# Kernel tuning notes

Hardware: AMD Instinct MI355X
Metric: run time of the kernel (lower is better)

Reference implementation:

```python
import jax, jax.numpy as jnp
import numpy as np

HEAD_DIM = 64
SCALE = HEAD_DIM ** -0.5
NUM_HEADS = 16


def setup_inputs() -> dict:
    key = jax.random.key(0)
    k1, k2, k3, k4 = jax.random.split(key, 4)
    dim = 1024
    query = jax.random.normal(k1, (8, 512, dim), dtype=jnp.float32)
    memory = jax.random.normal(k2, (8, 512, dim), dtype=jnp.float32)
    # nn.Linear weights are [out, in]; scale like default init
    W_Q = jax.random.normal(k3, (dim, dim), dtype=jnp.float32) * (dim ** -0.5)
    W_K = jax.random.normal(k4, (dim, dim), dtype=jnp.float32) * (dim ** -0.5)
    return {"query": query, "memory": memory, "W_Q": W_Q, "W_K": W_K}


def reference(query, memory, W_Q, W_K):
    # Q: [K, Lq, E], K: [B, Lk, E]  (E = H * D)
    Q = query @ W_Q.T
    Km = memory @ W_K.T
    Kb, Lq, E = Q.shape
    Bb, Lk, _ = Km.shape
    Qh = Q.reshape(Kb, Lq, NUM_HEADS, HEAD_DIM).transpose(0, 2, 1, 3)  # K H q D
    Kh = Km.reshape(Bb, Lk, NUM_HEADS, HEAD_DIM).transpose(0, 2, 1, 3)  # B H k D
    # logits: [B, K, H, q, k]
    logits = jnp.einsum('ahqd,bhkd->bahqk', Qh, Kh) * SCALE
    energies = jax.nn.logsumexp(logits, axis=-2) / SCALE  # [B, K, H, k]
    energies = energies.mean(axis=1)  # [B, H, k]
    return energies
```

## Files before the change

### kernel.cpp

```cpp
#include <hip/hip_runtime.h>
#include <hip/hip_bf16.h>

typedef short short8 __attribute__((ext_vector_type(8)));
typedef float f32x4 __attribute__((ext_vector_type(4)));
typedef unsigned short u16;

__device__ __forceinline__ unsigned short f2bf(float f) {
  unsigned int u = __float_as_uint(f);
  u += 0x7fffu + ((u >> 16) & 1u);
  return (unsigned short)(u >> 16);
}

__device__ __forceinline__ void glds16(const void* g, void* l) {
  __builtin_amdgcn_global_load_lds(
      (const __attribute__((address_space(1))) unsigned int*)g,
      (__attribute__((address_space(3))) unsigned int*)l, 16, 0, 0);
}

__device__ __forceinline__ void drain_then_sync() {
  __builtin_amdgcn_s_waitcnt(0);
  __syncthreads();
}

__global__ __launch_bounds__(256) void prep(const float4* __restrict__ q,
                                            const float4* __restrict__ m,
                                            const float4* __restrict__ wq,
                                            const float4* __restrict__ wk,
                                            ushort4* __restrict__ qb,
                                            ushort4* __restrict__ mb,
                                            ushort4* __restrict__ wqb,
                                            ushort4* __restrict__ wkb,
                                            float4* __restrict__ out0) {
  const int i = blockIdx.x * 256 + threadIdx.x;
  const float c = 0.18033688011112042f;
  if (i < 1048576) {
    float4 v = q[i];
    ushort4 o; o.x = f2bf(v.x); o.y = f2bf(v.y); o.z = f2bf(v.z); o.w = f2bf(v.w);
    qb[i] = o;
  } else if (i < 2097152) {
    float4 v = m[i - 1048576];
    ushort4 o; o.x = f2bf(v.x); o.y = f2bf(v.y); o.z = f2bf(v.z); o.w = f2bf(v.w);
    mb[i - 1048576] = o;
  } else if (i < 2359296) {
    float4 v = wq[i - 2097152];
    ushort4 o; o.x = f2bf(v.x * c); o.y = f2bf(v.y * c); o.z = f2bf(v.z * c); o.w = f2bf(v.w * c);
    wqb[i - 2097152] = o;
  } else if (i < 2621440) {
    float4 v = wk[i - 2359296];
    ushort4 o; o.x = f2bf(v.x); o.y = f2bf(v.y); o.z = f2bf(v.z); o.w = f2bf(v.w);
    wkb[i - 2359296] = o;
  } else if (i < 2637824) {
    out0[i - 2621440] = (float4){0.f, 0.f, 0.f, 0.f};
  }
}

__global__ __launch_bounds__(512) void gemm_db(const u16* __restrict__ A0,
                                               const u16* __restrict__ B0,
                                               u16* __restrict__ C0,
                                               const u16* __restrict__ A1,
                                               const u16* __restrict__ B1,
                                               u16* __restrict__ C1) {
  __shared__ u16 As[2][128 * 64];
  __shared__ u16 Bs[2][128 * 64];
  const int zz = blockIdx.x & 1;
  const u16* A = zz ? A1 : A0;
  const u16* B = zz ? B1 : B0;
  u16* C = zz ? C1 : C0;
  const int t = threadIdx.x;
  const int lane = t & 63, wave = t >> 6;
  const int l15 = lane & 15, quad = lane >> 4;
  const int mb = (blockIdx.x >> 1) * 128;
  const int nb = blockIdx.y * 128;
  const int wm = (wave & 1) * 64;
  const int wn = (wave >> 1) * 32;

  const int srow = lane >> 3;
  const int scol = ((lane & 7) ^ srow) * 8;
  const int sw = l15 & 7;

  f32x4 acc[4][2];
#pragma unroll
  for (int i = 0; i < 4; i++)
#pragma unroll
    for (int j = 0; j < 2; j++) acc[i][j] = (f32x4){0.f, 0.f, 0.f, 0.f};

#pragma unroll
  for (int j = 0; j < 2; j++) {
    const int g = wave * 2 + j;
    glds16(A + (size_t)(mb + g * 8 + srow) * 1024 + scol, &As[0][g * 512 + lane * 8]);
    glds16(B + (size_t)(nb + g * 8 + srow) * 1024 + scol, &Bs[0][g * 512 + lane * 8]);
  }

  for (int it = 0; it < 16; ++it) {
    drain_then_sync();
    if (it < 15) {
      const int kb = (it + 1) * 64, bf_ = (it + 1) & 1;
#pragma unroll
      for (int j = 0; j < 2; j++) {
        const int g = wave * 2 + j;
        glds16(A + (size_t)(mb + g * 8 + srow) * 1024 + kb + scol, &As[bf_][g * 512 + lane * 8]);
        glds16(B + (size_t)(nb + g * 8 + srow) * 1024 + kb + scol, &Bs[bf_][g * 512 + lane * 8]);
      }
    }
    const u16* as = As[it & 1];
    const u16* bs = Bs[it & 1];
#pragma unroll
    for (int kk = 0; kk < 2; kk++) {
      const int cb = kk * 4;
      short8 af[4], bfr[2];
#pragma unroll
      for (int mi = 0; mi < 4; mi++)
        af[mi] = *(const short8*)&as[(wm + mi * 16 + l15) * 64 + ((cb + quad) ^ sw) * 8];
#pragma unroll
      for (int ni = 0; ni < 2; ni++)
        bfr[ni] = *(const short8*)&bs[(wn + ni * 16 + l15) * 64 + ((cb + quad) ^ sw) * 8];
#pragma unroll
      for (int mi = 0; mi < 4; mi++)
#pragma unroll
        for (int ni = 0; ni < 2; ni++)
          acc[mi][ni] = __builtin_amdgcn_mfma_f32_16x16x32_bf16(
              af[mi], bfr[ni], acc[mi][ni], 0, 0, 0);
    }
  }

#pragma unroll
  for (int mi = 0; mi < 4; mi++)
#pragma unroll
    for (int r = 0; r < 4; r++) {
      const int row = mb + wm + mi * 16 + quad * 4 + r;
      const size_t base = (size_t)row * 1024 + nb + wn;
#pragma unroll
      for (int ni = 0; ni < 2; ni++)
        C[base + ni * 16 + l15] = f2bf(acc[mi][ni][r]);
    }
}

__global__ __launch_bounds__(256) void attn_lse2(const u16* __restrict__ Qp,
                                                 const u16* __restrict__ Kp,
                                                 float* __restrict__ out) {
  __shared__ u16 qs[2][64 * 64];
  const int t = threadIdx.x;
  const int lane = t & 63, wave = t >> 6;
  const int l15 = lane & 15, quad = lane >> 4;
  const int kt = blockIdx.x & 1, aa = blockIdx.x >> 1;
  const int h = blockIdx.y, b = blockIdx.z;
  const int kwave = kt * 256 + wave * 64;

  short8 klo[4], khi[4];
#pragma unroll
  for (int tt = 0; tt < 4; tt++) {
    const short8* kg = (const short8*)(Kp + (size_t)(b * 512 + kwave + tt * 16 + l15) * 1024
                                       + h * 64 + quad * 8);
    klo[tt] = kg[0];
    khi[tt] = kg[4];
  }

  const int srow = lane >> 3;
  const int scol = ((lane & 7) ^ srow) * 8;
  const u16* qbase = Qp + (size_t)(aa * 512) * 1024 + h * 64;

  const int sw = l15 & 7;
  const int colLo = (quad ^ sw) * 8;
  const int colHi = ((4 + quad) ^ sw) * 8;
  const int rrow = l15 * 64;

  float cs0 = 0.f, cs1 = 0.f, cs2 = 0.f, cs3 = 0.f;

#pragma unroll
  for (int j = 0; j < 2; j++) {
    const int mi_ = wave * 2 + j;
    glds16(qbase + (size_t)(mi_ * 8 + srow) * 1024 + scol, &qs[0][mi_ * 512 + lane * 8]);
  }

  for (int i = 0; i < 8; i++) {
    drain_then_sync();
    if (i < 7) {
#pragma unroll
      for (int j = 0; j < 2; j++) {
        const int mi_ = wave * 2 + j;
        glds16(qbase + (size_t)((i + 1) * 64 + mi_ * 8 + srow) * 1024 + scol,
               &qs[(i + 1) & 1][mi_ * 512 + lane * 8]);
      }
    }
    const u16* buf = qs[i & 1];
#pragma unroll
    for (int qt = 0; qt < 4; qt++) {
      short8 alo = *(const short8*)&buf[qt * 1024 + rrow + colLo];
      short8 ahi = *(const short8*)&buf[qt * 1024 + rrow + colHi];
      f32x4 ac0 = (f32x4){0.f, 0.f, 0.f, 0.f};
      f32x4 ac1 = ac0, ac2 = ac0, ac3 = ac0;
      ac0 = __builtin_amdgcn_mfma_f32_16x16x32_bf16(alo, klo[0], ac0, 0, 0, 0);
      ac0 = __builtin_amdgcn_mfma_f32_16x16x32_bf16(ahi, khi[0], ac0, 0, 0, 0);
      ac1 = __builtin_amdgcn_mfma_f32_16x16x32_bf16(alo, klo[1], ac1, 0, 0, 0);
      ac1 = __builtin_amdgcn_mfma_f32_16x16x32_bf16(ahi, khi[1], ac1, 0, 0, 0);
      ac2 = __builtin_amdgcn_mfma_f32_16x16x32_bf16(alo, klo[2], ac2, 0, 0, 0);
      ac2 = __builtin_amdgcn_mfma_f32_16x16x32_bf16(ahi, khi[2], ac2, 0, 0, 0);
      ac3 = __builtin_amdgcn_mfma_f32_16x16x32_bf16(alo, klo[3], ac3, 0, 0, 0);
      ac3 = __builtin_amdgcn_mfma_f32_16x16x32_bf16(ahi, khi[3], ac3, 0, 0, 0);
#pragma unroll
      for (int r = 0; r < 4; r++) {
        cs0 += __builtin_amdgcn_exp2f(ac0[r]);
        cs1 += __builtin_amdgcn_exp2f(ac1[r]);
        cs2 += __builtin_amdgcn_exp2f(ac2[r]);
        cs3 += __builtin_amdgcn_exp2f(ac3[r]);
      }
    }
  }
  cs0 += __shfl_xor(cs0, 16); cs0 += __shfl_xor(cs0, 32);
  cs1 += __shfl_xor(cs1, 16); cs1 += __shfl_xor(cs1, 32);
  cs2 += __shfl_xor(cs2, 16); cs2 += __shfl_xor(cs2, 32);
  cs3 += __shfl_xor(cs3, 16); cs3 += __shfl_xor(cs3, 32);
  const float v = quad == 0 ? cs0 : quad == 1 ? cs1 : quad == 2 ? cs2 : cs3;
  atomicAdd(out + (size_t)b * 8192 + h * 512 + kwave + quad * 16 + l15, __logf(v));
}

extern "C" void kernel_launch(void* const* d_in, const int* in_sizes, int n_in,
                              void* d_out, int out_size, void* d_ws, size_t ws_size,
                              hipStream_t stream) {
  const float* query  = (const float*)d_in[0];
  const float* memory = (const float*)d_in[1];
  const float* wq     = (const float*)d_in[2];
  const float* wk     = (const float*)d_in[3];
  float* out = (float*)d_out;

  char* ws = (char*)d_ws;
  const size_t MB = 1024 * 1024;
  u16* qb  = (u16*)(ws);
  u16* mb_ = (u16*)(ws + 8  * MB);
  u16* wqb = (u16*)(ws + 16 * MB);
  u16* wkb = (u16*)(ws + 18 * MB);
  u16* Qp  = (u16*)(ws + 20 * MB);
  u16* Kp  = (u16*)(ws + 28 * MB);

  prep<<<10304, 256, 0, stream>>>((const float4*)query, (const float4*)memory,
                                  (const float4*)wq, (const float4*)wk,
                                  (ushort4*)qb, (ushort4*)mb_, (ushort4*)wqb,
                                  (ushort4*)wkb, (float4*)d_out);
  gemm_db<<<dim3(64, 8), 512, 0, stream>>>(qb, wqb, Qp, mb_, wkb, Kp);
  attn_lse2<<<dim3(16, 16, 8), 256, 0, stream>>>(Qp, Kp, out);
}
```

Measured before the change: 147.3 us.

## Load Q in two 256-row chunks instead of double-buffered 64-row tiles

Replaces the 8-step double-buffered 64-row Q pipeline with two phases. Each phase loads 256 Q rows into a 32KB LDS buffer, waits once, then computes. This cuts the number of barriers and waitcnt drains from eight to two, but it loses the overlap between loads and compute within each phase and quadruples LDS use per block, which may lower occupancy. The exp accumulators are also split into four independent lanes per column to break the serial add dependency chain.

```diff
diff --git a/kernel.cpp b/kernel.cpp
--- a/kernel.cpp
+++ b/kernel.cpp
@@ -138,7 +138,7 @@
 __global__ __launch_bounds__(256) void attn_lse2(const u16* __restrict__ Qp,
                                                  const u16* __restrict__ Kp,
                                                  float* __restrict__ out) {
-  __shared__ u16 qs[2][64 * 64];
+  __shared__ u16 qs[256 * 64];
   const int t = threadIdx.x;
   const int lane = t & 63, wave = t >> 6;
   const int l15 = lane & 15, quad = lane >> 4;
@@ -164,48 +164,49 @@
   const int colHi = ((4 + quad) ^ sw) * 8;
   const int rrow = l15 * 64;
 
-  float cs0 = 0.f, cs1 = 0.f, cs2 = 0.f, cs3 = 0.f;
-
-#pragma unroll
-  for (int j = 0; j < 2; j++) {
-    const int mi_ = wave * 2 + j;
-    glds16(qbase + (size_t)(mi_ * 8 + srow) * 1024 + scol, &qs[0][mi_ * 512 + lane * 8]);
-  }
-
-  for (int i = 0; i < 8; i++) {
+  f32x4 csv0 = (f32x4){0.f, 0.f, 0.f, 0.f};
+  f32x4 csv1 = csv0, csv2 = csv0, csv3 = csv0;
+
+  for (int s = 0; s < 2; ++s) {
+    if (s) __syncthreads();
+#pragma unroll
+    for (int j = 0; j < 8; ++j) {
+      const int g = wave * 8 + j;
+      glds16(qbase + (size_t)(s * 256 + g * 8 + srow) * 1024 + scol,
+             &qs[g * 512 + lane * 8]);
+    }
     drain_then_sync();
-    if (i < 7) {
-#pragma unroll
-      for (int j = 0; j < 2; j++) {
-        const int mi_ = wave * 2 + j;
-        glds16(qbase + (size_t)((i + 1) * 64 + mi_ * 8 + srow) * 1024 + scol,
-               &qs[(i + 1) & 1][mi_ * 512 + lane * 8]);
+
+    for (int ii = 0; ii < 4; ++ii) {
+      const u16* buf = qs + ii * 4096;
+#pragma unroll
+      for (int qt = 0; qt < 4; ++qt) {
+        short8 alo = *(const short8*)&buf[qt * 1024 + rrow + colLo];
+        short8 ahi = *(const short8*)&buf[qt * 1024 + rrow + colHi];
+        f32x4 ac0 = (f32x4){0.f, 0.f, 0.f, 0.f};
+        f32x4 ac1 = ac0, ac2 = ac0, ac3 = ac0;
+        ac0 = __builtin_amdgcn_mfma_f32_16x16x32_bf16(alo, klo[0], ac0, 0, 0, 0);
+        ac0 = __builtin_amdgcn_mfma_f32_16x16x32_bf16(ahi, khi[0], ac0, 0, 0, 0);
+        ac1 = __builtin_amdgcn_mfma_f32_16x16x32_bf16(alo, klo[1], ac1, 0, 0, 0);
+        ac1 = __builtin_amdgcn_mfma_f32_16x16x32_bf16(ahi, khi[1], ac1, 0, 0, 0);
+        ac2 = __builtin_amdgcn_mfma_f32_16x16x32_bf16(alo, klo[2], ac2, 0, 0, 0);
+        ac2 = __builtin_amdgcn_mfma_f32_16x16x32_bf16(ahi, khi[2], ac2, 0, 0, 0);
+        ac3 = __builtin_amdgcn_mfma_f32_16x16x32_bf16(alo, klo[3], ac3, 0, 0, 0);
+        ac3 = __builtin_amdgcn_mfma_f32_16x16x32_bf16(ahi, khi[3], ac3, 0, 0, 0);
+#pragma unroll
+        for (int r = 0; r < 4; r++) {
+          csv0[r] += __builtin_amdgcn_exp2f(ac0[r]);
+          csv1[r] += __builtin_amdgcn_exp2f(ac1[r]);
+          csv2[r] += __builtin_amdgcn_exp2f(ac2[r]);
+          csv3[r] += __builtin_amdgcn_exp2f(ac3[r]);
+        }
       }
     }
-    const u16* buf = qs[i & 1];
-#pragma unroll
-    for (int qt = 0; qt < 4; qt++) {
-      short8 alo = *(const short8*)&buf[qt * 1024 + rrow + colLo];
-      short8 ahi = *(const short8*)&buf[qt * 1024 + rrow + colHi];
-      f32x4 ac0 = (f32x4){0.f, 0.f, 0.f, 0.f};
-      f32x4 ac1 = ac0, ac2 = ac0, ac3 = ac0;
-      ac0 = __builtin_amdgcn_mfma_f32_16x16x32_bf16(alo, klo[0], ac0, 0, 0, 0);
-      ac0 = __builtin_amdgcn_mfma_f32_16x16x32_bf16(ahi, khi[0], ac0, 0, 0, 0);
-      ac1 = __builtin_amdgcn_mfma_f32_16x16x32_bf16(alo, klo[1], ac1, 0, 0, 0);
-      ac1 = __builtin_amdgcn_mfma_f32_16x16x32_bf16(ahi, khi[1], ac1, 0, 0, 0);
-      ac2 = __builtin_amdgcn_mfma_f32_16x16x32_bf16(alo, klo[2], ac2, 0, 0, 0);
-      ac2 = __builtin_amdgcn_mfma_f32_16x16x32_bf16(ahi, khi[2], ac2, 0, 0, 0);
-      ac3 = __builtin_amdgcn_mfma_f32_16x16x32_bf16(alo, klo[3], ac3, 0, 0, 0);
-      ac3 = __builtin_amdgcn_mfma_f32_16x16x32_bf16(ahi, khi[3], ac3, 0, 0, 0);
-#pragma unroll
-      for (int r = 0; r < 4; r++) {
-        cs0 += __builtin_amdgcn_exp2f(ac0[r]);
-        cs1 += __builtin_amdgcn_exp2f(ac1[r]);
-        cs2 += __builtin_amdgcn_exp2f(ac2[r]);
-        cs3 += __builtin_amdgcn_exp2f(ac3[r]);
-      }
-    }
-  }
+  }
+  float cs0 = csv0[0] + csv0[1] + csv0[2] + csv0[3];
+  float cs1 = csv1[0] + csv1[1] + csv1[2] + csv1[3];
+  float cs2 = csv2[0] + csv2[1] + csv2[2] + csv2[3];
+  float cs3 = csv3[0] + csv3[1] + csv3[2] + csv3[3];
   cs0 += __shfl_xor(cs0, 16); cs0 += __shfl_xor(cs0, 32);
   cs1 += __shfl_xor(cs1, 16); cs1 += __shfl_xor(cs1, 32);
   cs2 += __shfl_xor(cs2, 16); cs2 += __shfl_xor(cs2, 32);
```

Result: slower. 165.7 us (+12.5%).

## Triple-buffer GEMM LDS with K=32 stages and partial vmcnt waits

Applied to the files above, without the earlier changes.

The projection GEMM now uses three LDS buffers of K=32 tiles instead of two K=64 buffers, with loads issued two stages ahead. A counted s_waitcnt vmcnt(2) replaces the full drain before each barrier, so the next stage's global-to-LDS loads stay in flight while the current tile is computed. The LDS swizzle is reworked for the 32-column rows. The trade-off is twice as many barriers per K sweep and a fully unrolled 32-iteration loop that adds code size and register pressure.

```diff
diff --git a/kernel.cpp b/kernel.cpp
--- a/kernel.cpp
+++ b/kernel.cpp
@@ -60,8 +60,8 @@
                                                const u16* __restrict__ A1,
                                                const u16* __restrict__ B1,
                                                u16* __restrict__ C1) {
-  __shared__ u16 As[2][128 * 64];
-  __shared__ u16 Bs[2][128 * 64];
+  __shared__ u16 As[3][128 * 32];
+  __shared__ u16 Bs[3][128 * 32];
   const int zz = blockIdx.x & 1;
   const u16* A = zz ? A1 : A0;
   const u16* B = zz ? B1 : B0;
@@ -74,9 +74,14 @@
   const int wm = (wave & 1) * 64;
   const int wn = (wave >> 1) * 32;
 
-  const int srow = lane >> 3;
-  const int scol = ((lane & 7) ^ srow) * 8;
-  const int sw = l15 & 7;
+  const int srow = lane >> 2;
+  const int sq = (lane & 3) ^ (srow & 3) ^ ((srow >> 2) & 3);
+  const size_t arow = (size_t)(mb + wave * 16 + srow) * 1024 + sq * 8;
+  const size_t brow = (size_t)(nb + wave * 16 + srow) * 1024 + sq * 8;
+  const int ldst = wave * 512 + lane * 8;
+
+  const int sw2 = (l15 & 3) ^ ((l15 >> 2) & 3);
+  const int rcol = (quad ^ sw2) * 8;
 
   f32x4 acc[4][2];
 #pragma unroll
@@ -84,43 +89,37 @@
 #pragma unroll
     for (int j = 0; j < 2; j++) acc[i][j] = (f32x4){0.f, 0.f, 0.f, 0.f};
 
-#pragma unroll
-  for (int j = 0; j < 2; j++) {
-    const int g = wave * 2 + j;
-    glds16(A + (size_t)(mb + g * 8 + srow) * 1024 + scol, &As[0][g * 512 + lane * 8]);
-    glds16(B + (size_t)(nb + g * 8 + srow) * 1024 + scol, &Bs[0][g * 512 + lane * 8]);
-  }
-
-  for (int it = 0; it < 16; ++it) {
-    drain_then_sync();
-    if (it < 15) {
-      const int kb = (it + 1) * 64, bf_ = (it + 1) & 1;
-#pragma unroll
-      for (int j = 0; j < 2; j++) {
-        const int g = wave * 2 + j;
-        glds16(A + (size_t)(mb + g * 8 + srow) * 1024 + kb + scol, &As[bf_][g * 512 + lane * 8]);
-        glds16(B + (size_t)(nb + g * 8 + srow) * 1024 + kb + scol, &Bs[bf_][g * 512 + lane * 8]);
-      }
-    }
-    const u16* as = As[it & 1];
-    const u16* bs = Bs[it & 1];
-#pragma unroll
-    for (int kk = 0; kk < 2; kk++) {
-      const int cb = kk * 4;
-      short8 af[4], bfr[2];
-#pragma unroll
-      for (int mi = 0; mi < 4; mi++)
-        af[mi] = *(const short8*)&as[(wm + mi * 16 + l15) * 64 + ((cb + quad) ^ sw) * 8];
+  glds16(A + arow, &As[0][ldst]);
+  glds16(B + brow, &Bs[0][ldst]);
+  glds16(A + arow + 32, &As[1][ldst]);
+  glds16(B + brow + 32, &Bs[1][ldst]);
+
+#pragma unroll
+  for (int it = 0; it < 32; ++it) {
+    if (it != 31) asm volatile("s_waitcnt vmcnt(2)" ::: "memory");
+    else          asm volatile("s_waitcnt vmcnt(0)" ::: "memory");
+    __builtin_amdgcn_s_barrier();
+    __builtin_amdgcn_sched_barrier(0);
+    if (it <= 29) {
+      const int bf_ = (it + 2) % 3;
+      glds16(A + arow + (size_t)(it + 2) * 32, &As[bf_][ldst]);
+      glds16(B + brow + (size_t)(it + 2) * 32, &Bs[bf_][ldst]);
+    }
+    const u16* as = As[it % 3];
+    const u16* bs = Bs[it % 3];
+    short8 af[4], bfr[2];
+#pragma unroll
+    for (int mi = 0; mi < 4; mi++)
+      af[mi] = *(const short8*)&as[(wm + mi * 16 + l15) * 32 + rcol];
+#pragma unroll
+    for (int ni = 0; ni < 2; ni++)
+      bfr[ni] = *(const short8*)&bs[(wn + ni * 16 + l15) * 32 + rcol];
+#pragma unroll
+    for (int mi = 0; mi < 4; mi++)
 #pragma unroll
       for (int ni = 0; ni < 2; ni++)
-        bfr[ni] = *(const short8*)&bs[(wn + ni * 16 + l15) * 64 + ((cb + quad) ^ sw) * 8];
-#pragma unroll
-      for (int mi = 0; mi < 4; mi++)
-#pragma unroll
-        for (int ni = 0; ni < 2; ni++)
-          acc[mi][ni] = __builtin_amdgcn_mfma_f32_16x16x32_bf16(
-              af[mi], bfr[ni], acc[mi][ni], 0, 0, 0);
-    }
+        acc[mi][ni] = __builtin_amdgcn_mfma_f32_16x16x32_bf16(
+            af[mi], bfr[ni], acc[mi][ni], 0, 0, 0);
   }
 
 #pragma unroll
```

Result: slower. 151.8 us (+3.0%).
